# Kernel tuning notes

Measured on AMD Instinct MI355X. Metric: run time of the kernel, lower is better.

Reference implementation:

```python
import jax, jax.numpy as jnp
import numpy as np

N, E, H, C, L, D, OUT = 50000, 800000, 4, 32, 3, 128, 64
EPS = 1e-5


def setup_inputs() -> dict:
    key = jax.random.key(0)
    ks = jax.random.split(key, 16)
    s = 1.0 / np.sqrt(D)
    return {
        "x": jax.random.normal(ks[0], (N, D), jnp.float32),
        "edge_index": jax.random.randint(ks[1], (2, E), 0, N, dtype=jnp.int32),
        "Wq": jax.random.normal(ks[2], (L, D, H * C), jnp.float32) * s,
        "bq": jax.random.normal(ks[3], (L, H * C), jnp.float32) * 0.02,
        "Wk": jax.random.normal(ks[4], (L, D, H * C), jnp.float32) * s,
        "bk": jax.random.normal(ks[5], (L, H * C), jnp.float32) * 0.02,
        "Wv": jax.random.normal(ks[6], (L, D, H * C), jnp.float32) * s,
        "bv": jax.random.normal(ks[7], (L, H * C), jnp.float32) * 0.02,
        "Ws": jax.random.normal(ks[8], (L, D, H * C), jnp.float32) * s,
        "bs": jax.random.normal(ks[9], (L, H * C), jnp.float32) * 0.02,
        "bn_g": jnp.ones((L, H * C), jnp.float32),
        "bn_b": jnp.zeros((L, H * C), jnp.float32),
        "W_out": jax.random.normal(ks[10], (D, OUT), jnp.float32) * s,
        "b_out": jax.random.normal(ks[11], (OUT,), jnp.float32) * 0.02,
        "bno_g": jnp.ones((OUT,), jnp.float32),
        "bno_b": jnp.zeros((OUT,), jnp.float32),
    }


def _batch_norm(x, g, b):
    # training-mode BatchNorm1d: per-feature batch mean/var (biased), eps=1e-5
    mu = x.mean(axis=0)
    var = x.var(axis=0)
    return g * (x - mu) * jax.lax.rsqrt(var + EPS) + b


def _transformer_conv(x, src, dst, Wq, bq, Wk, bk, Wv, bv, Ws, bs):
    n = x.shape[0]
    q = (x @ Wq + bq).reshape(n, H, C)  # query at target nodes
    k = (x @ Wk + bk).reshape(n, H, C)
    v = (x @ Wv + bv).reshape(n, H, C)
    # per-edge attention logits [E, H]
    score = (q[dst] * k[src]).sum(-1) / jnp.sqrt(jnp.float32(C))
    # numerically-stable softmax over incoming edges of each target node
    m = jax.ops.segment_max(score, dst, num_segments=n)
    ex = jnp.exp(score - m[dst])
    denom = jax.ops.segment_sum(ex, dst, num_segments=n)
    alpha = ex / denom[dst]  # [E, H]
    agg = jax.ops.segment_sum(v[src] * alpha[..., None], dst, num_segments=n)
    out = agg.reshape(n, H * C) + x @ Ws + bs  # concat heads + root/skip term
    return out


def reference(x, edge_index, Wq, bq, Wk, bk, Wv, bv, Ws, bs, bn_g, bn_b,
              W_out, b_out, bno_g, bno_b):
    src, dst = edge_index[0], edge_index[1]
    h = x
    for i in range(L):
        h = _transformer_conv(h, src, dst, Wq[i], bq[i], Wk[i], bk[i],
                              Wv[i], bv[i], Ws[i], bs[i])
        h = _batch_norm(h, bn_g[i], bn_b[i])
        h = jax.nn.relu(h)
    h = h @ W_out + b_out
    h = _batch_norm(h, bno_g, bno_b)
    return jax.nn.relu(h)
```

## Files before the change

### kernel.cpp

```cpp
#include <hip/hip_runtime.h>
#include <hip/hip_bf16.h>
#include <math.h>

#define D_FEAT 128
#define NLAYER 3
#define BN_EPS 1e-5f
#define INV_SQRT_C 0.17677669529663687f
#define SORT_NPB 1024
#define NREP 8
#define TP 136

typedef __bf16 bf16x8 __attribute__((ext_vector_type(8)));
typedef float f32x4 __attribute__((ext_vector_type(4)));

static __device__ __forceinline__ unsigned short f2bf(float f) {
    return __builtin_bit_cast(unsigned short, __float2bfloat16(f));
}
static __device__ __forceinline__ float bfl(unsigned u) { return __uint_as_float(u << 16); }
static __device__ __forceinline__ float bfh(unsigned u) { return __uint_as_float(u & 0xffff0000u); }
static __device__ __forceinline__ unsigned packbf(float a, float b) {
    return (unsigned)f2bf(a) | ((unsigned)f2bf(b) << 16);
}


__global__ void prep_kernel(const float* __restrict__ x, unsigned short* __restrict__ xb,
                            size_t n4,
                            const float* __restrict__ Wq, const float* __restrict__ Wk,
                            const float* __restrict__ Wv, const float* __restrict__ Ws,
                            const float* __restrict__ Wo,
                            unsigned short* __restrict__ Wt, unsigned short* __restrict__ Wot)
{
    const int CVTB = 1792;
    int b = blockIdx.x;
    if (b < CVTB) {
        for (size_t t = (size_t)b * blockDim.x + threadIdx.x; t < n4;
             t += (size_t)CVTB * blockDim.x) {
            size_t i = t * 4;
            float4 v = *(const float4*)(x + i);
            ushort4 u;
            u.x = f2bf(v.x); u.y = f2bf(v.y); u.z = f2bf(v.z); u.w = f2bf(v.w);
            *(ushort4*)(xb + i) = u;
        }
    } else {
        const int permat = 16384;
        const int main_total = NLAYER * 4 * permat;
        const int total = main_total + 64 * 128;
        const int WB = gridDim.x - CVTB;
        for (int i = (b - CVTB) * blockDim.x + threadIdx.x; i < total;
             i += WB * blockDim.x) {
            if (i < main_total) {
                int l = i / (4 * permat);
                int rem = i - l * (4 * permat);
                int mat = rem / permat;
                int e = rem - mat * permat;
                int nn = e >> 7;
                int kk = e & 127;
                const float* src = (mat == 0) ? Wq : (mat == 1) ? Wk : (mat == 2) ? Wv : Ws;
                Wt[(size_t)l * 4 * permat + mat * permat + nn * 128 + kk] =
                    f2bf(src[(size_t)l * permat + kk * 128 + nn]);
            } else {
                int e = i - main_total;
                int nn = e >> 7;
                int kk = e & 127;
                Wot[nn * 128 + kk] = f2bf(Wo[kk * 64 + nn]);
            }
        }
    }
}


__global__ void hist_kernel(const int* __restrict__ dst, int E, int* __restrict__ deg) {
    int e = blockIdx.x * blockDim.x + threadIdx.x;
    if (e < E) atomicAdd(&deg[dst[e]], 1);
}

__global__ __launch_bounds__(256) void scan1_kernel(const int* __restrict__ deg, int n,
                                                    int* __restrict__ rowptr,
                                                    int* __restrict__ partials) {
    int b = blockIdx.x, tid = threadIdx.x;
    int base = b * 1024 + tid * 4;
    int4 d = {0, 0, 0, 0};
    if (base + 3 < n) d = *(const int4*)(deg + base);
    else {
        if (base + 0 < n) d.x = deg[base + 0];
        if (base + 1 < n) d.y = deg[base + 1];
        if (base + 2 < n) d.z = deg[base + 2];
        if (base + 3 < n) d.w = deg[base + 3];
    }
    int p0 = d.x, p1 = p0 + d.y, p2 = p1 + d.z, p3 = p2 + d.w;
    int v = p3;
    int lane = tid & 63;
    #pragma unroll
    for (int off = 1; off < 64; off <<= 1) {
        int t = __shfl_up(v, off);
        if (lane >= off) v += t;
    }
    __shared__ int wsum[4];
    int w = tid >> 6;
    if (lane == 63) wsum[w] = v;
    __syncthreads();
    int woff = 0;
    #pragma unroll
    for (int j = 0; j < 4; ++j) if (j < w) woff += wsum[j];
    int excl = woff + v - p3;
    if (base + 0 < n) rowptr[base + 1] = excl + p0;
    if (base + 1 < n) rowptr[base + 2] = excl + p1;
    if (base + 2 < n) rowptr[base + 3] = excl + p2;
    if (base + 3 < n) rowptr[base + 4] = excl + p3;
    if (tid == 255) partials[b] = excl + p3;
    if (b == 0 && tid == 0) rowptr[0] = 0;
}

__global__ void scan2_kernel(int* __restrict__ partials, int nb) {
    int lane = threadIdx.x;
    int v = (lane < nb) ? partials[lane] : 0;
    #pragma unroll
    for (int off = 1; off < 64; off <<= 1) {
        int t = __shfl_up(v, off);
        if (lane >= off) v += t;
    }
    if (lane < nb) partials[lane] = v;
}

__global__ __launch_bounds__(256) void scan3_hist_kernel(
    int* __restrict__ rowptr, int n, const int* __restrict__ partials,
    int B, int* __restrict__ bhist)
{
    __shared__ int h[256];
    __shared__ int oldv[SORT_NPB];
    int b = blockIdx.x, tid = threadIdx.x;
    h[tid] = 0;
    int off = (b == 0) ? 0 : partials[b - 1];
    #pragma unroll
    for (int j = 0; j < SORT_NPB / 256; ++j) {
        int loc = j * 256 + tid;
        int i = b * SORT_NPB + loc;
        oldv[loc] = (i < n) ? rowptr[i + 1] : 0;
    }
    __syncthreads();
    #pragma unroll
    for (int j = 0; j < SORT_NPB / 256; ++j) {
        int loc = j * 256 + tid;
        int i = b * SORT_NPB + loc;
        if (i < n) {
            int d = (loc == 0) ? oldv[0] : (oldv[loc] - oldv[loc - 1]);
            if (d > 255) d = 255;
            atomicAdd(&h[255 - d], 1);
            rowptr[i + 1] = oldv[loc] + off;
        }
    }
    __syncthreads();
    bhist[tid * B + b] = h[tid];
}

__global__ void scatter_kernel(const int* __restrict__ src, const int* __restrict__ dst, int E,
                               const int* __restrict__ rowptr, int* __restrict__ cursor,
                               int* __restrict__ csrsrc) {
    int e = blockIdx.x * blockDim.x + threadIdx.x;
    if (e < E) {
        int d = dst[e];
        int p = atomicAdd(&cursor[d], 1);
        csrsrc[rowptr[d] + p] = src[e];
    }
}

__global__ __launch_bounds__(256) void bin_colscan_kernel(
    int* __restrict__ bhist, int B, int* __restrict__ binoff)
{
    int d = threadIdx.x;
    int run = 0;
    for (int b = 0; b < B; ++b) {
        int c = bhist[d * B + b];
        bhist[d * B + b] = run;
        run += c;
    }
    __shared__ int sd[256];
    sd[d] = run;
    __syncthreads();
    int v = run;
    for (int s = 1; s < 256; s <<= 1) {
        int t = (d >= s) ? sd[d - s] : 0;
        __syncthreads();
        sd[d] += t;
        __syncthreads();
    }
    binoff[d] = sd[d] - v;
}

__global__ __launch_bounds__(256) void bin_order_kernel(
    const int* __restrict__ rowptr, int n, int B,
    const int* __restrict__ bhist, const int* __restrict__ binoff,
    int* __restrict__ order)
{
    __shared__ int cur[256];
    int b = blockIdx.x, tid = threadIdx.x;
    cur[tid] = binoff[tid] + bhist[tid * B + b];
    __syncthreads();
    #pragma unroll
    for (int j = 0; j < SORT_NPB / 256; ++j) {
        int i = b * SORT_NPB + j * 256 + tid;
        if (i < n) {
            int d = rowptr[i + 1] - rowptr[i];
            if (d > 255) d = 255;
            int pos = atomicAdd(&cur[255 - d], 1);
            order[pos] = i;
        }
    }
}


__global__ __launch_bounds__(256, 2) void gemm_qkvs_kernel(
    const unsigned short* __restrict__ A,
    const float* __restrict__ stats, const float* __restrict__ g,
    const float* __restrict__ bb, int mode, int M,
    const unsigned short* __restrict__ Wt,
    const float* __restrict__ b0, const float* __restrict__ b1,
    const float* __restrict__ b2, const float* __restrict__ b3,
    unsigned short* __restrict__ q, unsigned short* __restrict__ kv,
    unsigned short* __restrict__ s)
{
    __shared__ float scale[128], shift[128];
    __shared__ unsigned short tile[128 * TP];
    int r0 = blockIdx.x * 128;
    int tid = threadIdx.x;
    int wid = tid >> 6, lane = tid & 63;
    int wm = wid >> 1, wn = wid & 1;
    int lr = lane & 15, lk = lane >> 4;

    if (mode && tid < 128) {
        float ssum = 0.f, qsum = 0.f;
        #pragma unroll
        for (int r = 0; r < NREP; ++r) {
            ssum += stats[r * 1024 + tid];
            qsum += stats[r * 1024 + 512 + tid];
        }
        float invN = 1.0f / (float)M;
        float mu = ssum * invN;
        float var = qsum * invN - mu * mu;
        float sc = rsqrtf(var + BN_EPS) * g[tid];
        scale[tid] = sc;
        shift[tid] = bb[tid] - mu * sc;
    }
    __syncthreads();

    bf16x8 a[4][4];
    #pragma unroll
    for (int ks = 0; ks < 4; ++ks) {
        int ko = ks * 32 + lk * 8;
        #pragma unroll
        for (int mi = 0; mi < 4; ++mi) {
            int arow = r0 + wm * 64 + mi * 16 + lr;
            int4 t = {0, 0, 0, 0};
            if (arow < M) t = *(const int4*)(A + (size_t)arow * 128 + ko);
            if (mode) {
                float4 sc0 = *(const float4*)&scale[ko];
                float4 sc1 = *(const float4*)&scale[ko + 4];
                float4 sh0 = *(const float4*)&shift[ko];
                float4 sh1 = *(const float4*)&shift[ko + 4];
                float v0 = fmaxf(bfl(t.x) * sc0.x + sh0.x, 0.f);
                float v1 = fmaxf(bfh(t.x) * sc0.y + sh0.y, 0.f);
                float v2 = fmaxf(bfl(t.y) * sc0.z + sh0.z, 0.f);
                float v3 = fmaxf(bfh(t.y) * sc0.w + sh0.w, 0.f);
                float v4 = fmaxf(bfl(t.z) * sc1.x + sh1.x, 0.f);
                float v5 = fmaxf(bfh(t.z) * sc1.y + sh1.y, 0.f);
                float v6 = fmaxf(bfl(t.w) * sc1.z + sh1.z, 0.f);
                float v7 = fmaxf(bfh(t.w) * sc1.w + sh1.w, 0.f);
                t.x = (int)packbf(v0, v1); t.y = (int)packbf(v2, v3);
                t.z = (int)packbf(v4, v5); t.w = (int)packbf(v6, v7);
            }
            a[mi][ks] = __builtin_bit_cast(bf16x8, t);
        }
    }

    #pragma unroll
    for (int cc = 0; cc < 2; ++cc) {
        int ct = blockIdx.y * 2 + cc;
        const unsigned short* W = Wt + (size_t)ct * 16384;

        f32x4 acc[4][4] = {};
        #pragma unroll
        for (int ks = 0; ks < 4; ++ks) {
            int ko = ks * 32 + lk * 8;
            bf16x8 b[4];
            #pragma unroll
            for (int nj = 0; nj < 4; ++nj) {
                int4 t = *(const int4*)(W + (size_t)(wn * 64 + nj * 16 + lr) * 128 + ko);
                b[nj] = __builtin_bit_cast(bf16x8, t);
            }
            #pragma unroll
            for (int mi = 0; mi < 4; ++mi)
                #pragma unroll
                for (int nj = 0; nj < 4; ++nj)
                    acc[mi][nj] = __builtin_amdgcn_mfma_f32_16x16x32_bf16(
                        a[mi][ks], b[nj], acc[mi][nj], 0, 0, 0);
        }

        const float* bias = (ct == 0) ? b0 : (ct == 1) ? b1 : (ct == 2) ? b2 : b3;
        __syncthreads();
        #pragma unroll
        for (int mi = 0; mi < 4; ++mi) {
            #pragma unroll
            for (int nj = 0; nj < 4; ++nj) {
                int col = wn * 64 + nj * 16 + lr;
                float bv = bias[col];
                #pragma unroll
                for (int reg = 0; reg < 4; ++reg) {
                    int rloc = wm * 64 + mi * 16 + lk * 4 + reg;
                    tile[rloc * TP + col] = f2bf(acc[mi][nj][reg] + bv);
                }
            }
        }
        __syncthreads();
        #pragma unroll
        for (int it = 0; it < 8; ++it) {
            int flat = (it * 256 + tid) * 8;
            int row = flat >> 7, col = flat & 127;
            int rw = r0 + row;
            if (rw < M) {
                int4 v = *(const int4*)&tile[row * TP + col];
                if (ct == 0) *(int4*)(q + (size_t)rw * 128 + col) = v;
                else if (ct == 1) *(int4*)(kv + (size_t)rw * 256 + col) = v;
                else if (ct == 2) *(int4*)(kv + (size_t)rw * 256 + 128 + col) = v;
                else *(int4*)(s + (size_t)rw * 128 + col) = v;
            }
        }
    }
}

__global__ __launch_bounds__(256, 2) void gemm_final_kernel(
    const unsigned short* __restrict__ A,
    const float* __restrict__ stats, const float* __restrict__ g,
    const float* __restrict__ bb, int M,
    const unsigned short* __restrict__ Wot, const float* __restrict__ bias,
    float* __restrict__ out, float* __restrict__ statsOut)
{
    __shared__ float scale[128], shift[128];
    __shared__ float fs[64], fq[64];
    int r0 = blockIdx.x * 128;
    int tid = threadIdx.x;
    int wid = tid >> 6, lane = tid & 63;
    int wm = wid >> 1, wn = wid & 1;
    int lr = lane & 15, lk = lane >> 4;

    if (tid < 128) {
        float ssum = 0.f, qsum = 0.f;
        #pragma unroll
        for (int r = 0; r < NREP; ++r) {
            ssum += stats[r * 1024 + tid];
            qsum += stats[r * 1024 + 512 + tid];
        }
        float invN = 1.0f / (float)M;
        float mu = ssum * invN;
        float var = qsum * invN - mu * mu;
        float sc = rsqrtf(var + BN_EPS) * g[tid];
        scale[tid] = sc;
        shift[tid] = bb[tid] - mu * sc;
    }
    if (tid < 64) { fs[tid] = 0.f; fq[tid] = 0.f; }
    __syncthreads();

    bf16x8 a[4][4];
    #pragma unroll
    for (int ks = 0; ks < 4; ++ks) {
        int ko = ks * 32 + lk * 8;
        #pragma unroll
        for (int mi = 0; mi < 4; ++mi) {
            int arow = r0 + wm * 64 + mi * 16 + lr;
            int4 t = {0, 0, 0, 0};
            if (arow < M) t = *(const int4*)(A + (size_t)arow * 128 + ko);
            float4 sc0 = *(const float4*)&scale[ko];
            float4 sc1 = *(const float4*)&scale[ko + 4];
            float4 sh0 = *(const float4*)&shift[ko];
            float4 sh1 = *(const float4*)&shift[ko + 4];
            float v0 = fmaxf(bfl(t.x) * sc0.x + sh0.x, 0.f);
            float v1 = fmaxf(bfh(t.x) * sc0.y + sh0.y, 0.f);
            float v2 = fmaxf(bfl(t.y) * sc0.z + sh0.z, 0.f);
            float v3 = fmaxf(bfh(t.y) * sc0.w + sh0.w, 0.f);
            float v4 = fmaxf(bfl(t.z) * sc1.x + sh1.x, 0.f);
            float v5 = fmaxf(bfh(t.z) * sc1.y + sh1.y, 0.f);
            float v6 = fmaxf(bfl(t.w) * sc1.z + sh1.z, 0.f);
            float v7 = fmaxf(bfh(t.w) * sc1.w + sh1.w, 0.f);
            t.x = (int)packbf(v0, v1); t.y = (int)packbf(v2, v3);
            t.z = (int)packbf(v4, v5); t.w = (int)packbf(v6, v7);
            a[mi][ks] = __builtin_bit_cast(bf16x8, t);
        }
    }

    f32x4 acc[4][2] = {};
    #pragma unroll
    for (int ks = 0; ks < 4; ++ks) {
        int ko = ks * 32 + lk * 8;
        bf16x8 b[2];
        #pragma unroll
        for (int nj = 0; nj < 2; ++nj) {
            int4 t = *(const int4*)(Wot + (size_t)(wn * 32 + nj * 16 + lr) * 128 + ko);
            b[nj] = __builtin_bit_cast(bf16x8, t);
        }
        #pragma unroll
        for (int mi = 0; mi < 4; ++mi)
            #pragma unroll
            for (int nj = 0; nj < 2; ++nj)
                acc[mi][nj] = __builtin_amdgcn_mfma_f32_16x16x32_bf16(
                    a[mi][ks], b[nj], acc[mi][nj], 0, 0, 0);
    }

    float csum[2] = {0.f, 0.f}, csq[2] = {0.f, 0.f};
    #pragma unroll
    for (int mi = 0; mi < 4; ++mi) {
        #pragma unroll
        for (int nj = 0; nj < 2; ++nj) {
            int col = wn * 32 + nj * 16 + lr;
            float bv = bias[col];
            #pragma unroll
            for (int reg = 0; reg < 4; ++reg) {
                int rw = r0 + wm * 64 + mi * 16 + lk * 4 + reg;
                if (rw < M) {
                    float val = acc[mi][nj][reg] + bv;
                    out[(size_t)rw * 64 + col] = val;
                    csum[nj] += val;
                    csq[nj] += val * val;
                }
            }
        }
    }
    #pragma unroll
    for (int nj = 0; nj < 2; ++nj) {
        csum[nj] += __shfl_xor(csum[nj], 16);
        csum[nj] += __shfl_xor(csum[nj], 32);
        csq[nj]  += __shfl_xor(csq[nj], 16);
        csq[nj]  += __shfl_xor(csq[nj], 32);
    }
    if (lane < 16) {
        #pragma unroll
        for (int nj = 0; nj < 2; ++nj) {
            int col = wn * 32 + nj * 16 + lr;
            atomicAdd(&fs[col], csum[nj]);
            atomicAdd(&fq[col], csq[nj]);
        }
    }
    __syncthreads();
    if (tid < 64) atomicAdd(&statsOut[tid], fs[tid]);
    else if (tid < 128) atomicAdd(&statsOut[512 + tid - 64], fq[tid - 64]);
}


__global__ __launch_bounds__(256) void attn_kernel(
    const unsigned short* __restrict__ q, const unsigned short* __restrict__ kv,
    const unsigned short* __restrict__ sk,
    const int* __restrict__ rowptr, const int* __restrict__ csrsrc,
    const int* __restrict__ order,
    unsigned short* __restrict__ hnext, float* __restrict__ stats, int N)
{
    __shared__ float ls[128], lq2[128];
    int tid = threadIdx.x;
    if (tid < 128) { ls[tid] = 0.f; lq2[tid] = 0.f; }
    __syncthreads();

    int wave = (blockIdx.x * blockDim.x + tid) >> 6;
    int lane = tid & 63;
    int gl = lane & 15;
    int slot = wave * 4 + (lane >> 4);
    bool nv = slot < N;
    int n = nv ? order[slot] : 0;

    int r0 = rowptr[n], r1 = rowptr[n + 1];
    int deg = nv ? (r1 - r0) : 0;
    int dmax = deg;
    dmax = max(dmax, __shfl_xor(dmax, 16));
    dmax = max(dmax, __shfl_xor(dmax, 32));

    int4 qu = *(const int4*)(q + (size_t)n * 128 + gl * 8);
    float qf[8];
    qf[0] = bfl(qu.x); qf[1] = bfh(qu.x); qf[2] = bfl(qu.y); qf[3] = bfh(qu.y);
    qf[4] = bfl(qu.z); qf[5] = bfh(qu.z); qf[6] = bfl(qu.w); qf[7] = bfh(qu.w);

    float m = -INFINITY, ssum = 0.f;
    float acc[8] = {};

    for (int i = 0; i < dmax; i += 8) {
        int eidx[8];
        bool av[8];
        #pragma unroll
        for (int j = 0; j < 8; ++j) {
            av[j] = (i + j) < deg;
            int e = csrsrc[r0 + i + j];
            eidx[j] = av[j] ? e : 0;
        }
        int4 K[8], V[8];
        #pragma unroll
        for (int j = 0; j < 8; ++j) {
            const unsigned short* row = kv + (size_t)eidx[j] * 256 + gl * 8;
            K[j] = *(const int4*)(row);
            V[j] = *(const int4*)(row + 128);
        }
        float sc[8];
        #pragma unroll
        for (int j = 0; j < 8; ++j) {
            float p = qf[0] * bfl(K[j].x) + qf[1] * bfh(K[j].x)
                    + qf[2] * bfl(K[j].y) + qf[3] * bfh(K[j].y)
                    + qf[4] * bfl(K[j].z) + qf[5] * bfh(K[j].z)
                    + qf[6] * bfl(K[j].w) + qf[7] * bfh(K[j].w);
            p += __shfl_xor(p, 1);
            p += __shfl_xor(p, 2);
            sc[j] = av[j] ? p * INV_SQRT_C : -INFINITY;
        }
        float mn = m;
        #pragma unroll
        for (int j = 0; j < 8; ++j) mn = fmaxf(mn, sc[j]);
        if (mn > m) {
            float scale = __expf(m - mn);
            ssum *= scale;
            #pragma unroll
            for (int c = 0; c < 8; ++c) acc[c] *= scale;
            m = mn;
        }
        #pragma unroll
        for (int j = 0; j < 8; ++j) {
            float ej = av[j] ? __expf(sc[j] - m) : 0.f;
            ssum += ej;
            acc[0] += ej * bfl(V[j].x); acc[1] += ej * bfh(V[j].x);
            acc[2] += ej * bfl(V[j].y); acc[3] += ej * bfh(V[j].y);
            acc[4] += ej * bfl(V[j].z); acc[5] += ej * bfh(V[j].z);
            acc[6] += ej * bfl(V[j].w); acc[7] += ej * bfh(V[j].w);
        }
    }

    float o[8];
    if (nv) {
        float inv = (ssum > 0.f) ? 1.0f / ssum : 0.f;
        int4 su = *(const int4*)(sk + (size_t)n * 128 + gl * 8);
        o[0] = acc[0] * inv + bfl(su.x); o[1] = acc[1] * inv + bfh(su.x);
        o[2] = acc[2] * inv + bfl(su.y); o[3] = acc[3] * inv + bfh(su.y);
        o[4] = acc[4] * inv + bfl(su.z); o[5] = acc[5] * inv + bfh(su.z);
        o[6] = acc[6] * inv + bfl(su.w); o[7] = acc[7] * inv + bfh(su.w);
        int4 st;
        st.x = (int)packbf(o[0], o[1]); st.y = (int)packbf(o[2], o[3]);
        st.z = (int)packbf(o[4], o[5]); st.w = (int)packbf(o[6], o[7]);
        *(int4*)(hnext + (size_t)n * 128 + gl * 8) = st;
    } else {
        #pragma unroll
        for (int c = 0; c < 8; ++c) o[c] = 0.f;
    }

    float s8[8], q8[8];
    #pragma unroll
    for (int c = 0; c < 8; ++c) { s8[c] = o[c]; q8[c] = o[c] * o[c]; }
    #pragma unroll
    for (int c = 0; c < 8; ++c) {
        s8[c] += __shfl_xor(s8[c], 16); s8[c] += __shfl_xor(s8[c], 32);
        q8[c] += __shfl_xor(q8[c], 16); q8[c] += __shfl_xor(q8[c], 32);
    }
    if (lane < 16) {
        #pragma unroll
        for (int c = 0; c < 8; ++c) {
            atomicAdd(&ls[gl * 8 + c], s8[c]);
            atomicAdd(&lq2[gl * 8 + c], q8[c]);
        }
    }
    __syncthreads();
    float* srep = stats + (blockIdx.x & (NREP - 1)) * 1024;
    if (tid < 128) atomicAdd(&srep[tid], ls[tid]);
    else atomicAdd(&srep[512 + tid - 128], lq2[tid - 128]);
}


__global__ __launch_bounds__(256) void bn_apply_f32_kernel(
    const float* __restrict__ x, float* __restrict__ y,
    const float* __restrict__ stats, const float* __restrict__ g,
    const float* __restrict__ b, int N, int F)
{
    __shared__ float scale[128], shift[128];
    int tid = threadIdx.x;
    if (tid < F) {
        float invN = 1.0f / (float)N;
        float mu = stats[tid] * invN;
        float var = stats[512 + tid] * invN - mu * mu;
        float sc = rsqrtf(var + BN_EPS) * g[tid];
        scale[tid] = sc;
        shift[tid] = b[tid] - mu * sc;
    }
    __syncthreads();
    size_t total4 = (size_t)N * F >> 2;
    int Fm = F - 1;
    for (size_t t = (size_t)blockIdx.x * blockDim.x + tid; t < total4;
         t += (size_t)gridDim.x * blockDim.x) {
        size_t i = t * 4;
        int f = (int)(i & (size_t)Fm);
        float4 v = *(const float4*)(x + i);
        float4 o;
        o.x = fmaxf(v.x * scale[f + 0] + shift[f + 0], 0.f);
        o.y = fmaxf(v.y * scale[f + 1] + shift[f + 1], 0.f);
        o.z = fmaxf(v.z * scale[f + 2] + shift[f + 2], 0.f);
        o.w = fmaxf(v.w * scale[f + 3] + shift[f + 3], 0.f);
        *(float4*)(y + i) = o;
    }
}


static inline size_t al16(size_t x) { return (x + 15) & ~(size_t)15; }

extern "C" void kernel_launch(void* const* d_in, const int* in_sizes, int n_in,
                              void* d_out, int out_size, void* d_ws, size_t ws_size,
                              hipStream_t stream) {
    const float* x    = (const float*)d_in[0];
    const int*   edge = (const int*)d_in[1];
    const float* Wq   = (const float*)d_in[2];
    const float* bq   = (const float*)d_in[3];
    const float* Wk   = (const float*)d_in[4];
    const float* bk   = (const float*)d_in[5];
    const float* Wv   = (const float*)d_in[6];
    const float* bv   = (const float*)d_in[7];
    const float* Wsk  = (const float*)d_in[8];
    const float* bsk  = (const float*)d_in[9];
    const float* bng  = (const float*)d_in[10];
    const float* bnb  = (const float*)d_in[11];
    const float* Wo   = (const float*)d_in[12];
    const float* bo   = (const float*)d_in[13];
    const float* bnog = (const float*)d_in[14];
    const float* bnob = (const float*)d_in[15];

    const int N = in_sizes[0] / D_FEAT;
    const int E = in_sizes[1] / 2;
    const int* esrc = edge;
    const int* edst = edge + E;

    const int SB = (N + SORT_NPB - 1) / SORT_NPB;
    const size_t STATS_F = (size_t)(NLAYER * NREP + 1) * 1024;

    char* wsb = (char*)d_ws;
    unsigned short* xb = (unsigned short*)wsb; wsb += al16((size_t)N * 128 * 2);
    unsigned short* kv = (unsigned short*)wsb; wsb += al16((size_t)N * 256 * 2);
    unsigned short* q  = (unsigned short*)wsb; wsb += al16((size_t)N * 128 * 2);
    unsigned short* s  = (unsigned short*)wsb; wsb += al16((size_t)N * 128 * 2);
    unsigned short* hnext = (unsigned short*)wsb; wsb += al16((size_t)N * 128 * 2);
    float* outpre = (float*)wsb; wsb += al16((size_t)N * 64 * 4);
    unsigned short* Wt  = (unsigned short*)wsb; wsb += al16((size_t)NLAYER * 4 * 16384 * 2);
    unsigned short* Wot = (unsigned short*)wsb; wsb += al16((size_t)64 * 128 * 2);
    float* stats  = (float*)wsb; wsb += al16(STATS_F * 4);
    int* deg      = (int*)wsb;   wsb += al16((size_t)N * 4);
    int* cursor   = (int*)wsb;   wsb += al16((size_t)N * 4);
    size_t zero_bytes = (char*)wsb - (char*)stats;
    int* rowptr   = (int*)wsb;   wsb += al16((size_t)(N + 1) * 4);
    int* csrsrc   = (int*)wsb;   wsb += al16((size_t)(E + 64) * 4);
    int* partials = (int*)wsb;   wsb += al16(256 * 4);
    int* bhist    = (int*)wsb;   wsb += al16((size_t)256 * SB * 4);
    int* binoff   = (int*)wsb;   wsb += al16(256 * 4);
    int* order    = (int*)wsb;   wsb += al16((size_t)N * 4);

    prep_kernel<<<2048, 256, 0, stream>>>(x, xb, (size_t)N * 128 / 4,
                                          Wq, Wk, Wv, Wsk, Wo, Wt, Wot);
    hipMemsetAsync(stats, 0, zero_bytes, stream);

    const int nb1 = (N + 1023) / 1024;
    hist_kernel<<<(E + 255) / 256, 256, 0, stream>>>(edst, E, deg);
    scan1_kernel<<<nb1, 256, 0, stream>>>(deg, N, rowptr, partials);
    scan2_kernel<<<1, 64, 0, stream>>>(partials, nb1);
    scan3_hist_kernel<<<SB, 256, 0, stream>>>(rowptr, N, partials, SB, bhist);
    scatter_kernel<<<(E + 255) / 256, 256, 0, stream>>>(esrc, edst, E, rowptr, cursor, csrsrc);
    bin_colscan_kernel<<<1, 256, 0, stream>>>(bhist, SB, binoff);
    bin_order_kernel<<<SB, 256, 0, stream>>>(rowptr, N, SB, bhist, binoff, order);

    const int gemm_rb = (N + 127) / 128;
    const int attn_blocks = (N + 15) / 16;
    const unsigned short* hin = xb;
    for (int l = 0; l < NLAYER; ++l) {
        const float* statsIn = (l == 0) ? (const float*)nullptr
                                        : stats + (size_t)(l - 1) * NREP * 1024;
        const float* gIn = (l == 0) ? (const float*)nullptr : bng + (l - 1) * 128;
        const float* bIn = (l == 0) ? (const float*)nullptr : bnb + (l - 1) * 128;
        gemm_qkvs_kernel<<<dim3(gemm_rb, 2), 256, 0, stream>>>(
            hin, statsIn, gIn, bIn, (l == 0) ? 0 : 1, N,
            Wt + (size_t)l * 4 * 16384,
            bq + l * 128, bk + l * 128, bv + l * 128, bsk + l * 128,
            q, kv, s);
        attn_kernel<<<attn_blocks, 256, 0, stream>>>(q, kv, s, rowptr, csrsrc, order,
                                                     hnext, stats + (size_t)l * NREP * 1024, N);
        hin = hnext;
    }

    float* fstats = stats + (size_t)NLAYER * NREP * 1024;
    gemm_final_kernel<<<gemm_rb, 256, 0, stream>>>(
        hnext, stats + (size_t)2 * NREP * 1024, bng + 2 * 128, bnb + 2 * 128, N,
        Wot, bo, outpre, fstats);
    bn_apply_f32_kernel<<<2048, 256, 0, stream>>>(outpre, (float*)d_out, fstats,
                                                  bnog, bnob, N, 64);
}
```

Measured before the change: 446.8 us.

## Double-buffer edge K/V gathers in attention and fuse degree histogram into prep

The attention loop now prefetches the next chunk of 8 neighbor K/V rows into a second register buffer while the current chunk is being scored and accumulated, so gather latency can overlap with compute. Separately, the degree histogram is folded into the prep kernel as extra blocks, which removes one launch and lets it run alongside the bf16 conversion. The memset now runs before prep so deg is zeroed in time. Doubling the K/V register buffers raises register pressure, which may lower occupancy in the attention kernel.

Result: slower. 585.4 us (+31.0%).

```diff
diff --git a/kernel.cpp b/kernel.cpp
--- a/kernel.cpp
+++ b/kernel.cpp
@@ -28,9 +28,11 @@
                             const float* __restrict__ Wq, const float* __restrict__ Wk,
                             const float* __restrict__ Wv, const float* __restrict__ Ws,
                             const float* __restrict__ Wo,
-                            unsigned short* __restrict__ Wt, unsigned short* __restrict__ Wot)
+                            unsigned short* __restrict__ Wt, unsigned short* __restrict__ Wot,
+                            const int* __restrict__ edst, int E, int* __restrict__ deg)
 {
     const int CVTB = 1792;
+    const int WEND = 2048;
     int b = blockIdx.x;
     if (b < CVTB) {
         for (size_t t = (size_t)b * blockDim.x + threadIdx.x; t < n4;
@@ -41,11 +43,11 @@
             u.x = f2bf(v.x); u.y = f2bf(v.y); u.z = f2bf(v.z); u.w = f2bf(v.w);
             *(ushort4*)(xb + i) = u;
         }
-    } else {
+    } else if (b < WEND) {
         const int permat = 16384;
         const int main_total = NLAYER * 4 * permat;
         const int total = main_total + 64 * 128;
-        const int WB = gridDim.x - CVTB;
+        const int WB = WEND - CVTB;
         for (int i = (b - CVTB) * blockDim.x + threadIdx.x; i < total;
              i += WB * blockDim.x) {
             if (i < main_total) {
@@ -65,14 +67,12 @@
                 Wot[nn * 128 + kk] = f2bf(Wo[kk * 64 + nn]);
             }
         }
-    }
-}
-
-
-__global__ void hist_kernel(const int* __restrict__ dst, int E, int* __restrict__ deg) {
-    int e = blockIdx.x * blockDim.x + threadIdx.x;
-    if (e < E) atomicAdd(&deg[dst[e]], 1);
-}
+    } else {
+        int e = (b - WEND) * blockDim.x + threadIdx.x;
+        if (e < E) atomicAdd(&deg[edst[e]], 1);
+    }
+}
+
 
 __global__ __launch_bounds__(256) void scan1_kernel(const int* __restrict__ deg, int n,
                                                     int* __restrict__ rowptr,
@@ -444,6 +444,55 @@
 }
 
 
+#define LOADCHUNK(IO, K_, V_)                                              \
+    {                                                                      \
+        int io_ = (IO);                                                    \
+        _Pragma("unroll")                                                  \
+        for (int j = 0; j < 8; ++j) {                                      \
+            bool av_ = (io_ + j) < deg;                                    \
+            int e_ = csrsrc[r0 + io_ + j];                                 \
+            e_ = av_ ? e_ : 0;                                             \
+            const unsigned short* row_ = kv + (size_t)e_ * 256 + gl * 8;   \
+            K_[j] = *(const int4*)(row_);                                  \
+            V_[j] = *(const int4*)(row_ + 128);                            \
+        }                                                                  \
+    }
+
+#define COMPUTECHUNK(IO, K_, V_)                                           \
+    {                                                                      \
+        int io_ = (IO);                                                    \
+        float sc[8];                                                       \
+        _Pragma("unroll")                                                  \
+        for (int j = 0; j < 8; ++j) {                                      \
+            float p = qf[0] * bfl(K_[j].x) + qf[1] * bfh(K_[j].x)          \
+                    + qf[2] * bfl(K_[j].y) + qf[3] * bfh(K_[j].y)          \
+                    + qf[4] * bfl(K_[j].z) + qf[5] * bfh(K_[j].z)          \
+                    + qf[6] * bfl(K_[j].w) + qf[7] * bfh(K_[j].w);         \
+            p += __shfl_xor(p, 1);                                         \
+            p += __shfl_xor(p, 2);                                         \
+            sc[j] = ((io_ + j) < deg) ? p * INV_SQRT_C : -INFINITY;        \
+        }                                                                  \
+        float mn = m;                                                      \
+        _Pragma("unroll")                                                  \
+        for (int j = 0; j < 8; ++j) mn = fmaxf(mn, sc[j]);                 \
+        if (mn > m) {                                                      \
+            float scl = __expf(m - mn);                                    \
+            ssum *= scl;                                                   \
+            _Pragma("unroll")                                              \
+            for (int c = 0; c < 8; ++c) acc[c] *= scl;                     \
+            m = mn;                                                        \
+        }                                                                  \
+        _Pragma("unroll")                                                  \
+        for (int j = 0; j < 8; ++j) {                                      \
+            float ej = ((io_ + j) < deg) ? __expf(sc[j] - m) : 0.f;        \
+            ssum += ej;                                                    \
+            acc[0] += ej * bfl(V_[j].x); acc[1] += ej * bfh(V_[j].x);      \
+            acc[2] += ej * bfl(V_[j].y); acc[3] += ej * bfh(V_[j].y);      \
+            acc[4] += ej * bfl(V_[j].z); acc[5] += ej * bfh(V_[j].z);      \
+            acc[6] += ej * bfl(V_[j].w); acc[7] += ej * bfh(V_[j].w);      \
+        }                                                                  \
+    }
+
 __global__ __launch_bounds__(256) void attn_kernel(
     const unsigned short* __restrict__ q, const unsigned short* __restrict__ kv,
     const unsigned short* __restrict__ sk,
@@ -477,51 +526,19 @@
     float m = -INFINITY, ssum = 0.f;
     float acc[8] = {};
 
-    for (int i = 0; i < dmax; i += 8) {
-        int eidx[8];
-        bool av[8];
-        #pragma unroll
-        for (int j = 0; j < 8; ++j) {
-            av[j] = (i + j) < deg;
-            int e = csrsrc[r0 + i + j];
-            eidx[j] = av[j] ? e : 0;
-        }
-        int4 K[8], V[8];
-        #pragma unroll
-        for (int j = 0; j < 8; ++j) {
-            const unsigned short* row = kv + (size_t)eidx[j] * 256 + gl * 8;
-            K[j] = *(const int4*)(row);
-            V[j] = *(const int4*)(row + 128);
-        }
-        float sc[8];
-        #pragma unroll
-        for (int j = 0; j < 8; ++j) {
-            float p = qf[0] * bfl(K[j].x) + qf[1] * bfh(K[j].x)
-                    + qf[2] * bfl(K[j].y) + qf[3] * bfh(K[j].y)
-                    + qf[4] * bfl(K[j].z) + qf[5] * bfh(K[j].z)
-                    + qf[6] * bfl(K[j].w) + qf[7] * bfh(K[j].w);
-            p += __shfl_xor(p, 1);
-            p += __shfl_xor(p, 2);
-            sc[j] = av[j] ? p * INV_SQRT_C : -INFINITY;
-        }
-        float mn = m;
-        #pragma unroll
-        for (int j = 0; j < 8; ++j) mn = fmaxf(mn, sc[j]);
-        if (mn > m) {
-            float scale = __expf(m - mn);
-            ssum *= scale;
-            #pragma unroll
-            for (int c = 0; c < 8; ++c) acc[c] *= scale;
-            m = mn;
-        }
-        #pragma unroll
-        for (int j = 0; j < 8; ++j) {
-            float ej = av[j] ? __expf(sc[j] - m) : 0.f;
-            ssum += ej;
-            acc[0] += ej * bfl(V[j].x); acc[1] += ej * bfh(V[j].x);
-            acc[2] += ej * bfl(V[j].y); acc[3] += ej * bfh(V[j].y);
-            acc[4] += ej * bfl(V[j].z); acc[5] += ej * bfh(V[j].z);
-            acc[6] += ej * bfl(V[j].w); acc[7] += ej * bfh(V[j].w);
+    int4 Ka[8], Va[8], Kb[8], Vb[8];
+    if (dmax > 0) {
+        LOADCHUNK(0, Ka, Va);
+        int i = 0;
+        while (true) {
+            if (i + 8 < dmax) LOADCHUNK(i + 8, Kb, Vb);
+            COMPUTECHUNK(i, Ka, Va);
+            i += 8;
+            if (i >= dmax) break;
+            if (i + 8 < dmax) LOADCHUNK(i + 8, Ka, Va);
+            COMPUTECHUNK(i, Kb, Vb);
+            i += 8;
+            if (i >= dmax) break;
         }
     }
 
@@ -647,12 +664,13 @@
     int* binoff   = (int*)wsb;   wsb += al16(256 * 4);
     int* order    = (int*)wsb;   wsb += al16((size_t)N * 4);
 
-    prep_kernel<<<2048, 256, 0, stream>>>(x, xb, (size_t)N * 128 / 4,
-                                          Wq, Wk, Wv, Wsk, Wo, Wt, Wot);
     hipMemsetAsync(stats, 0, zero_bytes, stream);
+    const int prep_blocks = 2048 + (E + 255) / 256;
+    prep_kernel<<<prep_blocks, 256, 0, stream>>>(x, xb, (size_t)N * 128 / 4,
+                                                 Wq, Wk, Wv, Wsk, Wo, Wt, Wot,
+                                                 edst, E, deg);
 
     const int nb1 = (N + 1023) / 1024;
-    hist_kernel<<<(E + 255) / 256, 256, 0, stream>>>(edst, E, deg);
     scan1_kernel<<<nb1, 256, 0, stream>>>(deg, N, rowptr, partials);
     scan2_kernel<<<1, 64, 0, stream>>>(partials, nb1);
     scan3_hist_kernel<<<SB, 256, 0, stream>>>(rowptr, N, partials, SB, bhist);
```
